# Kernel optimization log

Measured on AMD Instinct MI355X. Metric: run time of the kernel, lower is better.

The kernel has to match this reference:

```python
import jax, jax.numpy as jnp
import numpy as np

DIM = 1024
NUM_HEADS = 16
HEAD_DIM = DIM // NUM_HEADS
WINDOW = 128
EPS = 1e-5


def setup_inputs() -> dict:
    key = jax.random.key(0)
    ks = jax.random.split(key, 8)
    B, S, D = 1, 2048, DIM
    x = jax.random.normal(ks[0], (B, S, D), dtype=jnp.float32)
    # xavier-uniform-ish scale for linear weights (torch layout: [out, in])
    def xavier(k, out_f, in_f):
        lim = np.sqrt(6.0 / (in_f + out_f)).astype(np.float32)
        return jax.random.uniform(k, (out_f, in_f), jnp.float32, -lim, lim)
    qkv_w = xavier(ks[1], 3 * D, D)
    out_w = xavier(ks[2], D, D)
    ln_g = jnp.ones((D,), jnp.float32)
    ln_b = jnp.zeros((D,), jnp.float32)
    w1 = xavier(ks[3], 4 * D, D)
    b1 = jnp.zeros((4 * D,), jnp.float32)
    w2 = xavier(ks[4], D, 4 * D)
    b2 = jnp.zeros((D,), jnp.float32)
    return {"x": x, "qkv_w": qkv_w, "out_w": out_w, "ln_g": ln_g,
            "ln_b": ln_b, "w1": w1, "b1": b1, "w2": w2, "b2": b2}


def reference(x, qkv_w, out_w, ln_g, ln_b, w1, b1, w2, b2):
    B, S, D = x.shape
    H, hd = NUM_HEADS, HEAD_DIM
    residual = x
    # LayerNorm (pre-norm)
    mu = jnp.mean(x, axis=-1, keepdims=True)
    var = jnp.var(x, axis=-1, keepdims=True)
    xn = (x - mu) * jax.lax.rsqrt(var + EPS) * ln_g + ln_b
    # QKV projection (torch Linear: y = x @ W^T)
    qkv = xn @ qkv_w.T                              # [B,S,3D]
    qkv = qkv.reshape(B, S, 3, H, hd).transpose(2, 0, 3, 1, 4)  # [3,B,H,S,hd]
    q, k, v = qkv[0], qkv[1], qkv[2]
    # Local-window boolean mask: |i - j| <= window_size // 2
    w = WINDOW // 2
    i = jnp.arange(S)[:, None]
    j = jnp.arange(S)[None, :]
    local_mask = jnp.abs(i - j) <= w                # [S,S]
    # SDPA with boolean mask
    scale = 1.0 / np.sqrt(hd).astype(np.float32)
    scores = jnp.einsum('bhqd,bhkd->bhqk', q, k) * scale
    scores = jnp.where(local_mask, scores, -jnp.inf)
    attn = jax.nn.softmax(scores, axis=-1)
    attn_out = jnp.einsum('bhqk,bhkd->bhqd', attn, v)
    attn_out = attn_out.transpose(0, 2, 1, 3).reshape(B, S, D)
    attn_out = attn_out @ out_w.T
    out = residual + attn_out
    # FFN (no second norm in this module), exact GELU
    h = jax.nn.gelu(out @ w1.T + b1, approximate=False)
    ffn_out = h @ w2.T + b2
    return out + ffn_out
```

## Files before the change

### kernel.cpp

```cpp
#include <hip/hip_runtime.h>
#include <math.h>

typedef unsigned short u16;
typedef __attribute__((ext_vector_type(8))) short short8;
typedef __attribute__((ext_vector_type(4))) float f32x4;
typedef __attribute__((ext_vector_type(4))) int i32x4;
typedef __attribute__((ext_vector_type(4))) u16 u16x4;

__device__ inline u16 f2bf(float f){
  union { float f; unsigned int u; } x; x.f = f;
  unsigned int r = x.u + 0x7fffu + ((x.u >> 16) & 1u);
  return (u16)(r >> 16);
}

__global__ __launch_bounds__(256) void prep_kernel(
    const float* __restrict__ x, const float* __restrict__ g, const float* __restrict__ b,
    u16* __restrict__ xn,
    const float* __restrict__ qkv_w, u16* __restrict__ qkvw_b,
    const float* __restrict__ out_w, u16* __restrict__ outw_b,
    const float* __restrict__ w1,    u16* __restrict__ w1_b,
    const float* __restrict__ w2,    u16* __restrict__ w2_b)
{
  const int tid = threadIdx.x;
  int bid = blockIdx.x;
  if (bid < 2048){
    const int row = bid;
    float4 v = *(const float4*)(x + (size_t)row*1024 + tid*4);
    float s  = v.x + v.y + v.z + v.w;
    float ss = v.x*v.x + v.y*v.y + v.z*v.z + v.w*v.w;
    #pragma unroll
    for (int off = 32; off; off >>= 1){
      s  += __shfl_xor(s,  off, 64);
      ss += __shfl_xor(ss, off, 64);
    }
    __shared__ float red[8];
    const int wid = tid >> 6;
    if ((tid & 63) == 0){ red[wid] = s; red[4+wid] = ss; }
    __syncthreads();
    float S  = red[0]+red[1]+red[2]+red[3];
    float SS = red[4]+red[5]+red[6]+red[7];
    float mu  = S * (1.0f/1024.0f);
    float var = SS * (1.0f/1024.0f) - mu*mu;
    float rs  = rsqrtf(var + 1e-5f);
    float4 gv = *(const float4*)(g + tid*4);
    float4 bv = *(const float4*)(b + tid*4);
    u16x4 pk;
    pk.x = f2bf((v.x-mu)*rs*gv.x + bv.x);
    pk.y = f2bf((v.y-mu)*rs*gv.y + bv.y);
    pk.z = f2bf((v.z-mu)*rs*gv.z + bv.z);
    pk.w = f2bf((v.w-mu)*rs*gv.w + bv.w);
    *(u16x4*)(xn + (size_t)row*1024 + tid*4) = pk;
    return;
  }
  bid -= 2048;
  const float* src; u16* dst;
  if (bid < 3072){ src = qkv_w; dst = qkvw_b; }
  else if (bid < 3072+1024){ src = out_w; dst = outw_b; bid -= 3072; }
  else if (bid < 3072+1024+4096){ src = w1; dst = w1_b; bid -= 3072+1024; }
  else { src = w2; dst = w2_b; bid -= 3072+1024+4096; }
  const size_t i = ((size_t)bid*256 + tid) * 4;
  float4 v = *(const float4*)(src + i);
  u16x4 pk;
  pk.x = f2bf(v.x); pk.y = f2bf(v.y); pk.z = f2bf(v.z); pk.w = f2bf(v.w);
  *(u16x4*)(dst + i) = pk;
}

template<int EPI, int BN>
__global__ __launch_bounds__(256) void gemm_lds(
    const u16* __restrict__ A, const u16* __restrict__ B,
    float* __restrict__ outF, u16* __restrict__ outB,
    const float* __restrict__ bias, const float* __restrict__ resid,
    int M, int N, int K, int nbx, int nwg, int Kc)
{
  constexpr int NR = BN / 32;
  __shared__ u16 As[2][128*64];
  __shared__ u16 Bs[2][BN*64];
  const int tid = threadIdx.x;
  const int l   = tid & 63;
  const int w   = tid >> 6;
  const int wr  = w >> 1, wc = w & 1;
  const int orig = blockIdx.x;
  const int wgid = (orig & 7) * (nwg >> 3) + (orig >> 3);
  const int bcol = wgid % nbx, brow = wgid / nbx;
  const int kz = blockIdx.y;
  const int l15 = l & 15, l4 = l >> 4;

  const u16* Ab = A + (size_t)brow*128*K + (size_t)kz*Kc;
  const u16* Bb = B + (size_t)bcol*BN*K  + (size_t)kz*Kc;

  f32x4 acc[4][NR];
  #pragma unroll
  for (int i = 0; i < 4; ++i)
    #pragma unroll
    for (int j = 0; j < NR; ++j)
      acc[i][j] = (f32x4){0.f, 0.f, 0.f, 0.f};

  const int rsub = l >> 3;
  const int csrc = ((l & 7) ^ rsub) * 8;
  const int swz  = (l15 & 7) * 8;
  const int nkt = Kc >> 6;

  auto stage = [&](int kt, int buf){
    const u16* Ag = Ab + kt*64 + csrc;
    const u16* Bg = Bb + kt*64 + csrc;
    #pragma unroll
    for (int i = 0; i < 4; ++i){
      const int ca = w*4 + i;
      __builtin_amdgcn_global_load_lds(
        (const __attribute__((address_space(1))) void*)(Ag + (size_t)(ca*8 + rsub)*K),
        (__attribute__((address_space(3))) void*)(&As[buf][ca*512]), 16, 0, 0);
    }
    #pragma unroll
    for (int i = 0; i < NR; ++i){
      const int cb = w*NR + i;
      __builtin_amdgcn_global_load_lds(
        (const __attribute__((address_space(1))) void*)(Bg + (size_t)(cb*8 + rsub)*K),
        (__attribute__((address_space(3))) void*)(&Bs[buf][cb*512]), 16, 0, 0);
    }
  };

  stage(0, 0);
  __syncthreads();
  for (int kt = 0; kt < nkt; ++kt){
    const int cur = kt & 1;
    if (kt + 1 < nkt) stage(kt + 1, cur ^ 1);
    #pragma unroll
    for (int ks = 0; ks < 2; ++ks){
      const int kop = (ks*32 + l4*8) ^ swz;
      short8 af[4], bfr[NR];
      #pragma unroll
      for (int i = 0; i < 4; ++i)  af[i]  = *(const short8*)&As[cur][(wr*64 + i*16 + l15)*64 + kop];
      #pragma unroll
      for (int j = 0; j < NR; ++j) bfr[j] = *(const short8*)&Bs[cur][(wc*(BN/2) + j*16 + l15)*64 + kop];
      #pragma unroll
      for (int i = 0; i < 4; ++i)
        #pragma unroll
        for (int j = 0; j < NR; ++j)
          acc[i][j] = __builtin_amdgcn_mfma_f32_16x16x32_bf16(af[i], bfr[j], acc[i][j], 0, 0, 0);
    }
    __syncthreads();
  }

  #pragma unroll
  for (int i = 0; i < 4; ++i){
    #pragma unroll
    for (int j = 0; j < NR; ++j){
      #pragma unroll
      for (int r = 0; r < 4; ++r){
        int row = brow*128 + wr*64 + i*16 + l4*4 + r;
        int col = bcol*BN + wc*(BN/2) + j*16 + l15;
        float v = acc[i][j][r];
        size_t o = (size_t)row * N + col;
        if constexpr (EPI == 0){
          outB[o] = f2bf(v);
        } else if constexpr (EPI == 1){
          v += resid[o];
          outF[o] = v;
          outB[o] = f2bf(v);
        } else if constexpr (EPI == 2){
          v += bias[col];
          v = 0.5f * v * (1.0f + erff(v * 0.70710678118654752f));
          outB[o] = f2bf(v);
        } else {
          outF[(size_t)kz * M * N + o] = v;
        }
      }
    }
  }
}

__global__ __launch_bounds__(256) void reduce_ffn2(const float* __restrict__ p,
                                                   const float* __restrict__ bias,
                                                   const float* __restrict__ resid,
                                                   float* __restrict__ out){
  const size_t s = (size_t)2048*1024;
  const size_t i = ((size_t)blockIdx.x * 256 + threadIdx.x) * 4;
  float4 a0 = *(const float4*)(p + i);
  float4 a1 = *(const float4*)(p + s + i);
  float4 a2 = *(const float4*)(p + 2*s + i);
  float4 a3 = *(const float4*)(p + 3*s + i);
  float4 r  = *(const float4*)(resid + i);
  float4 bb = *(const float4*)(bias + (i & 1023));
  float4 o;
  o.x = a0.x + a1.x + a2.x + a3.x + r.x + bb.x;
  o.y = a0.y + a1.y + a2.y + a3.y + r.y + bb.y;
  o.z = a0.z + a1.z + a2.z + a3.z + r.z + bb.z;
  o.w = a0.w + a1.w + a2.w + a3.w + r.w + bb.w;
  *(float4*)(out + i) = o;
}

__global__ __launch_bounds__(256) void attn_kernel(const u16* __restrict__ qkv, u16* __restrict__ attn_out){
  constexpr int S = 2048, D3 = 3072;
  const int qt = blockIdx.x, h = blockIdx.y;
  const int q0 = qt * 64;
  const int tid = threadIdx.x;
  const int l = tid & 63, w = tid >> 6;
  const int l15 = l & 15, l4 = l >> 4;

  __shared__ u16 smem[31232];
  u16 (*Qs)[72]  = (u16(*)[72]) (smem);
  u16 (*Ks)[72]  = (u16(*)[72]) (smem + 4608);
  u16 (*Ps)[200] = (u16(*)[200])(smem + 4608);
  u16 (*Vt)[200] = (u16(*)[200])(smem + 18432);

  #pragma unroll
  for (int i = 0; i < 2; ++i){
    int cid = tid + 256*i; int r = cid >> 3, c = cid & 7;
    *(i32x4*)&Qs[r][c*8] = *(const i32x4*)(qkv + (size_t)(q0 + r)*D3 + h*64 + c*8);
  }
  #pragma unroll
  for (int i = 0; i < 6; ++i){
    int cid = tid + 256*i; int r = cid >> 3, c = cid & 7;
    int kj = q0 - 64 + r;
    i32x4 kv = {0,0,0,0}, vv = {0,0,0,0};
    if (kj >= 0 && kj < S){
      kv = *(const i32x4*)(qkv + (size_t)kj*D3 + 1024 + h*64 + c*8);
      vv = *(const i32x4*)(qkv + (size_t)kj*D3 + 2048 + h*64 + c*8);
    }
    *(i32x4*)&Ks[r][c*8] = kv;
    union { i32x4 v; u16 u[8]; } uu; uu.v = vv;
    #pragma unroll
    for (int j = 0; j < 8; ++j) Vt[c*8 + j][r] = uu.u[j];
  }
  __syncthreads();

  f32x4 sc[12];
  #pragma unroll
  for (int cf = 0; cf < 12; ++cf) sc[cf] = (f32x4){0.f,0.f,0.f,0.f};
  const int ko = l4 * 8;
  short8 a0 = *(const short8*)&Qs[16*w + l15][ko];
  short8 a1 = *(const short8*)&Qs[16*w + l15][32 + ko];
  #pragma unroll
  for (int cf = 0; cf < 12; ++cf){
    short8 b0 = *(const short8*)&Ks[cf*16 + l15][ko];
    short8 b1 = *(const short8*)&Ks[cf*16 + l15][32 + ko];
    sc[cf] = __builtin_amdgcn_mfma_f32_16x16x32_bf16(a0, b0, sc[cf], 0, 0, 0);
    sc[cf] = __builtin_amdgcn_mfma_f32_16x16x32_bf16(a1, b1, sc[cf], 0, 0, 0);
  }
  __syncthreads();

  const float scale = 0.125f;
  #pragma unroll
  for (int r = 0; r < 4; ++r){
    const int qrl = 16*w + l4*4 + r;
    float mx = -1e30f;
    #pragma unroll
    for (int cf = 0; cf < 12; ++cf){
      int j  = cf*16 + l15;
      int kj = q0 - 64 + j;
      bool ok = (j >= qrl) && (j <= qrl + 128) && (kj >= 0) && (kj < S);
      float sv = ok ? sc[cf][r]*scale : -1e30f;
      sc[cf][r] = sv;
      mx = fmaxf(mx, sv);
    }
    #pragma unroll
    for (int off = 1; off < 16; off <<= 1) mx = fmaxf(mx, __shfl_xor(mx, off, 64));
    float sm = 0.f;
    #pragma unroll
    for (int cf = 0; cf < 12; ++cf){
      float pv = __expf(sc[cf][r] - mx);
      sc[cf][r] = pv;
      sm += pv;
    }
    #pragma unroll
    for (int off = 1; off < 16; off <<= 1) sm += __shfl_xor(sm, off, 64);
    float inv = 1.0f / sm;
    #pragma unroll
    for (int cf = 0; cf < 12; ++cf) Ps[qrl][cf*16 + l15] = f2bf(sc[cf][r] * inv);
  }
  __syncthreads();

  f32x4 o[4];
  #pragma unroll
  for (int df = 0; df < 4; ++df) o[df] = (f32x4){0.f,0.f,0.f,0.f};
  #pragma unroll
  for (int kk = 0; kk < 6; ++kk){
    short8 a = *(const short8*)&Ps[16*w + l15][kk*32 + ko];
    #pragma unroll
    for (int df = 0; df < 4; ++df){
      short8 b = *(const short8*)&Vt[df*16 + l15][kk*32 + ko];
      o[df] = __builtin_amdgcn_mfma_f32_16x16x32_bf16(a, b, o[df], 0, 0, 0);
    }
  }
  #pragma unroll
  for (int df = 0; df < 4; ++df){
    #pragma unroll
    for (int r = 0; r < 4; ++r){
      attn_out[(size_t)(q0 + 16*w + l4*4 + r)*1024 + h*64 + df*16 + l15] = f2bf(o[df][r]);
    }
  }
}

extern "C" void kernel_launch(void* const* d_in, const int* in_sizes, int n_in,
                              void* d_out, int out_size, void* d_ws, size_t ws_size,
                              hipStream_t stream)
{
  const float* x     = (const float*)d_in[0];
  const float* qkv_w = (const float*)d_in[1];
  const float* out_w = (const float*)d_in[2];
  const float* ln_g  = (const float*)d_in[3];
  const float* ln_b  = (const float*)d_in[4];
  const float* w1    = (const float*)d_in[5];
  const float* b1    = (const float*)d_in[6];
  const float* w2    = (const float*)d_in[7];
  const float* b2    = (const float*)d_in[8];
  float* out_final = (float*)d_out;

  char* p = (char*)d_ws;
  u16* xn_b   = (u16*)p; p += (size_t)2048*1024*2;
  u16* qkv_b  = (u16*)p; p += (size_t)2048*3072*2;
  u16* attn_b = (u16*)p; p += (size_t)2048*1024*2;
  u16* out_b  = (u16*)p; p += (size_t)2048*1024*2;
  u16* qkvw_b = (u16*)p; p += (size_t)3072*1024*2;
  u16* outw_b = (u16*)p; p += (size_t)1024*1024*2;
  u16* w1_b   = (u16*)p; p += (size_t)4096*1024*2;
  u16* w2_b   = (u16*)p; p += (size_t)1024*4096*2;
  float* out_f= (float*)p; p += (size_t)2048*1024*4;
  u16* h_b    = (u16*)p; p += (size_t)2048*4096*2;

  float* partials = (float*)xn_b;

  prep_kernel<<<14336, 256, 0, stream>>>(x, ln_g, ln_b, xn_b,
                                         qkv_w, qkvw_b, out_w, outw_b,
                                         w1, w1_b, w2, w2_b);
  gemm_lds<0,64><<<dim3(768), 256, 0, stream>>>(xn_b, qkvw_b, nullptr, qkv_b, nullptr, nullptr,
                                                2048, 3072, 1024, 48, 768, 1024);
  attn_kernel<<<dim3(32,16), 256, 0, stream>>>(qkv_b, attn_b);
  gemm_lds<1,64><<<dim3(256), 256, 0, stream>>>(attn_b, outw_b, out_f, out_b, nullptr, x,
                                                2048, 1024, 1024, 16, 256, 1024);
  gemm_lds<2,128><<<dim3(512), 256, 0, stream>>>(out_b, w1_b, nullptr, h_b, b1, nullptr,
                                                 2048, 4096, 1024, 32, 512, 1024);
  gemm_lds<4,128><<<dim3(128, 4), 256, 0, stream>>>(h_b, w2_b, partials, nullptr, nullptr, nullptr,
                                                    2048, 1024, 4096, 8, 128, 1024);
  reduce_ffn2<<<2048, 256, 0, stream>>>(partials, b2, out_f, out_final);
}
```

Before: 129.0 us.

## Deepen GEMM pipeline to 4-stage BK=32 ring with vmcnt-based waits

```diff
diff --git a/kernel.cpp b/kernel.cpp
--- a/kernel.cpp
+++ b/kernel.cpp
@@ -6,6 +6,9 @@
 typedef __attribute__((ext_vector_type(4))) float f32x4;
 typedef __attribute__((ext_vector_type(4))) int i32x4;
 typedef __attribute__((ext_vector_type(4))) u16 u16x4;
+
+#define AS1 __attribute__((address_space(1)))
+#define AS3 __attribute__((address_space(3)))
 
 __device__ inline u16 f2bf(float f){
   union { float f; unsigned int u; } x; x.f = f;
@@ -72,9 +75,12 @@
     const float* __restrict__ bias, const float* __restrict__ resid,
     int M, int N, int K, int nbx, int nwg, int Kc)
 {
-  constexpr int NR = BN / 32;
-  __shared__ u16 As[2][128*64];
-  __shared__ u16 Bs[2][BN*64];
+  constexpr int NR  = BN / 32;
+  constexpr int ACH = 2;
+  constexpr int BCH = BN / 64;
+  constexpr int L   = ACH + BCH;
+  __shared__ u16 As[4][128*32];
+  __shared__ u16 Bs[4][BN*32];
   const int tid = threadIdx.x;
   const int l   = tid & 63;
   const int w   = tid >> 6;
@@ -95,50 +101,50 @@
     for (int j = 0; j < NR; ++j)
       acc[i][j] = (f32x4){0.f, 0.f, 0.f, 0.f};
 
-  const int rsub = l >> 3;
-  const int csrc = ((l & 7) ^ rsub) * 8;
-  const int swz  = (l15 & 7) * 8;
-  const int nkt = Kc >> 6;
+  const int rsub = l >> 2;
+  const int csrc = ((l & 3) ^ ((l >> 3) & 3)) * 8;
+  const int kop  = ((l4 ^ ((l15 >> 1) & 3)) * 8);
+  const int nkt = Kc >> 5;
 
   auto stage = [&](int kt, int buf){
-    const u16* Ag = Ab + kt*64 + csrc;
-    const u16* Bg = Bb + kt*64 + csrc;
-    #pragma unroll
-    for (int i = 0; i < 4; ++i){
-      const int ca = w*4 + i;
+    const u16* Ag = Ab + kt*32 + csrc;
+    const u16* Bg = Bb + kt*32 + csrc;
+    #pragma unroll
+    for (int i = 0; i < ACH; ++i){
+      const int ca = w*ACH + i;
       __builtin_amdgcn_global_load_lds(
-        (const __attribute__((address_space(1))) void*)(Ag + (size_t)(ca*8 + rsub)*K),
-        (__attribute__((address_space(3))) void*)(&As[buf][ca*512]), 16, 0, 0);
-    }
-    #pragma unroll
-    for (int i = 0; i < NR; ++i){
-      const int cb = w*NR + i;
+        (const AS1 void*)(Ag + (size_t)(ca*16 + rsub)*K),
+        (AS3 void*)(&As[buf][ca*512]), 16, 0, 0);
+    }
+    #pragma unroll
+    for (int i = 0; i < BCH; ++i){
+      const int cb = w*BCH + i;
       __builtin_amdgcn_global_load_lds(
-        (const __attribute__((address_space(1))) void*)(Bg + (size_t)(cb*8 + rsub)*K),
-        (__attribute__((address_space(3))) void*)(&Bs[buf][cb*512]), 16, 0, 0);
+        (const AS1 void*)(Bg + (size_t)(cb*16 + rsub)*K),
+        (AS3 void*)(&Bs[buf][cb*512]), 16, 0, 0);
     }
   };
 
-  stage(0, 0);
-  __syncthreads();
+  stage(0, 0); stage(1, 1); stage(2, 2);
   for (int kt = 0; kt < nkt; ++kt){
-    const int cur = kt & 1;
-    if (kt + 1 < nkt) stage(kt + 1, cur ^ 1);
-    #pragma unroll
-    for (int ks = 0; ks < 2; ++ks){
-      const int kop = (ks*32 + l4*8) ^ swz;
-      short8 af[4], bfr[NR];
+    if (kt < nkt - 2)
+      asm volatile("s_waitcnt vmcnt(%0)\n\ts_barrier" :: "n"(2*L) : "memory");
+    else if (kt == nkt - 2)
+      asm volatile("s_waitcnt vmcnt(%0)\n\ts_barrier" :: "n"(L) : "memory");
+    else
+      asm volatile("s_waitcnt vmcnt(0)\n\ts_barrier" ::: "memory");
+    if (kt + 3 < nkt) stage(kt + 3, (kt + 3) & 3);
+    const int cur = kt & 3;
+    short8 af[4], bfr[NR];
+    #pragma unroll
+    for (int i = 0; i < 4; ++i)  af[i]  = *(const short8*)&As[cur][(wr*64 + i*16 + l15)*32 + kop];
+    #pragma unroll
+    for (int j = 0; j < NR; ++j) bfr[j] = *(const short8*)&Bs[cur][(wc*(BN/2) + j*16 + l15)*32 + kop];
+    #pragma unroll
+    for (int i = 0; i < 4; ++i)
       #pragma unroll
-      for (int i = 0; i < 4; ++i)  af[i]  = *(const short8*)&As[cur][(wr*64 + i*16 + l15)*64 + kop];
-      #pragma unroll
-      for (int j = 0; j < NR; ++j) bfr[j] = *(const short8*)&Bs[cur][(wc*(BN/2) + j*16 + l15)*64 + kop];
-      #pragma unroll
-      for (int i = 0; i < 4; ++i)
-        #pragma unroll
-        for (int j = 0; j < NR; ++j)
-          acc[i][j] = __builtin_amdgcn_mfma_f32_16x16x32_bf16(af[i], bfr[j], acc[i][j], 0, 0, 0);
-    }
-    __syncthreads();
+      for (int j = 0; j < NR; ++j)
+        acc[i][j] = __builtin_amdgcn_mfma_f32_16x16x32_bf16(af[i], bfr[j], acc[i][j], 0, 0, 0);
   }
 
   #pragma unroll
@@ -323,8 +329,8 @@
   prep_kernel<<<14336, 256, 0, stream>>>(x, ln_g, ln_b, xn_b,
                                          qkv_w, qkvw_b, out_w, outw_b,
                                          w1, w1_b, w2, w2_b);
-  gemm_lds<0,64><<<dim3(768), 256, 0, stream>>>(xn_b, qkvw_b, nullptr, qkv_b, nullptr, nullptr,
-                                                2048, 3072, 1024, 48, 768, 1024);
+  gemm_lds<0,128><<<dim3(384), 256, 0, stream>>>(xn_b, qkvw_b, nullptr, qkv_b, nullptr, nullptr,
+                                                 2048, 3072, 1024, 24, 384, 1024);
   attn_kernel<<<dim3(32,16), 256, 0, stream>>>(qkv_b, attn_b);
   gemm_lds<1,64><<<dim3(256), 256, 0, stream>>>(attn_b, outw_b, out_f, out_b, nullptr, x,
                                                 2048, 1024, 1024, 16, 256, 1024);
```

Result: slower. 147.0 us (+14.0%).
